# Optimization experiments

Measured on AMD Instinct MI355X. Metric: run time of the kernel, lower is better.

Reference implementation:

```python
import jax, jax.numpy as jnp
import numpy as np

H2 = 1.0  # self.bandwidth = bandwidth**2 with bandwidth=1.0

Q, N, D = 4096, 65536, 32


def setup_inputs() -> dict:
    key = jax.random.key(0)
    k1, k2, k3 = jax.random.split(key, 3)
    X = jax.random.normal(k1, (Q, D), dtype=jnp.float32)
    X_train = jax.random.normal(k2, (N, D), dtype=jnp.float32)
    sample_weight = jax.random.uniform(k3, (N,), dtype=jnp.float32)  # non-negative
    return {"X": X, "X_train": X_train, "sample_weight": sample_weight}


def reference(X, X_train, sample_weight):
    # Brute-force ('standard'/RootTree) KDE: every query sees all train points.
    d = X.shape[-1]
    d2 = (jnp.sum(X * X, axis=-1, keepdims=True)
          + jnp.sum(X_train * X_train, axis=-1)[None, :]
          - 2.0 * (X @ X_train.T))
    # GaussianKernel(diff) = (2*pi)^{-d/2} exp(-||diff||^2 / (2*H2))
    log_k = -0.5 * d2 / H2 - 0.5 * d * jnp.log(jnp.float32(2.0 * np.pi))
    # log( sum_j w_j K_ij / (bw_norm * sum_j w_j) ), bw_norm = H2**(d/2)
    log_num = jax.scipy.special.logsumexp(log_k + jnp.log(sample_weight)[None, :], axis=-1)
    log_norm = 0.5 * d * jnp.log(jnp.float32(H2)) + jnp.log(jnp.sum(sample_weight))
    return log_num - log_norm
```

## Files before the change

kernel.cpp:

```cpp
#include <hip/hip_runtime.h>
#include <math.h>

#define QN 4096
#define NN 65536
#define DD 32

typedef __attribute__((ext_vector_type(8))) _Float16 half8;
typedef __attribute__((ext_vector_type(4))) _Float16 half4v;
typedef __attribute__((ext_vector_type(4))) float floatx4;

#define LOG2E 1.4426950408889634f
#define HALF_D_LOG_2PI 29.40603306254953f

#define ASCALE 2954.6394357789634f
#define BSCALE 4096.0f
#define BIAS_F 1065353216.0f
#define CAPF   1585446912.0f
#define CENTER 0.970656f

__device__ __forceinline__ float fexp_term(float v) {
    v = __builtin_fminf(__builtin_fmaxf(v, 0.0f), CAPF);
    return __int_as_float((int)v);
}


__global__ __launch_bounds__(256) void prep_all(
    const float* __restrict__ X, const float* __restrict__ Xt,
    const float* __restrict__ w, _Float16* __restrict__ Xh,
    float* __restrict__ qn, _Float16* __restrict__ Xth,
    float* __restrict__ c, float* __restrict__ sumw) {
    const int b = blockIdx.x;
    if (b < 128) {
        int tid  = b * 256 + threadIdx.x;
        int row  = tid >> 3;
        int part = tid & 7;
        const float4 v = ((const float4*)X)[row * 8 + part];
        float nrm = v.x * v.x + v.y * v.y + v.z * v.z + v.w * v.w;
        nrm += __shfl_xor(nrm, 1);
        nrm += __shfl_xor(nrm, 2);
        nrm += __shfl_xor(nrm, 4);
        half4v h = { (_Float16)(v.x * ASCALE), (_Float16)(v.y * ASCALE),
                     (_Float16)(v.z * ASCALE), (_Float16)(v.w * ASCALE) };
        *(half4v*)(Xh + row * DD + part * 4) = h;
        if (part == 0) qn[row] = 0.5f * nrm;
    } else if (b < 2176) {
        int tid  = (b - 128) * 256 + threadIdx.x;
        int row  = tid >> 3;
        int part = tid & 7;
        const float4 v = ((const float4*)Xt)[row * 8 + part];
        float nrm = v.x * v.x + v.y * v.y + v.z * v.z + v.w * v.w;
        nrm += __shfl_xor(nrm, 1);
        nrm += __shfl_xor(nrm, 2);
        nrm += __shfl_xor(nrm, 4);
        half4v h = { (_Float16)(v.x * BSCALE), (_Float16)(v.y * BSCALE),
                     (_Float16)(v.z * BSCALE), (_Float16)(v.w * BSCALE) };
        *(half4v*)(Xth + row * DD + part * 4) = h;
        if (part == 0)
            c[row] = w[row] * __builtin_amdgcn_exp2f(-0.5f * LOG2E * nrm) * CENTER;
    } else {
        int bid = b - 2176;
        float v = 0.f;
        for (int i = bid * 256 + threadIdx.x; i < NN; i += 64 * 256)
            v += w[i];
        #pragma unroll
        for (int o = 1; o < 64; o <<= 1) v += __shfl_xor(v, o);
        __shared__ float red[4];
        if ((threadIdx.x & 63) == 0) red[threadIdx.x >> 6] = v;
        __syncthreads();
        if (threadIdx.x == 0) atomicAdd(sumw, red[0] + red[1] + red[2] + red[3]);
    }
}

__global__ __launch_bounds__(256) void kde_main(
    const _Float16* __restrict__ Xh, const _Float16* __restrict__ Xth,
    const float* __restrict__ c, float* __restrict__ S) {
    const int lane   = threadIdx.x & 63;
    const int wave   = threadIdx.x >> 6;
    const int quad   = lane >> 4;
    const int l16    = lane & 15;
    const int m_base = blockIdx.x * 256 + wave * 64;
    const int n_beg  = blockIdx.y * 512;

    half8 a0 = *(const half8*)(Xh + (m_base +  0 + l16) * DD + quad * 8);
    half8 a1 = *(const half8*)(Xh + (m_base + 16 + l16) * DD + quad * 8);
    half8 a2 = *(const half8*)(Xh + (m_base + 32 + l16) * DD + quad * 8);
    half8 a3 = *(const half8*)(Xh + (m_base + 48 + l16) * DD + quad * 8);

    float s0[4][4] = {};
    float s1[4][4] = {};
    const floatx4 cbias = {BIAS_F, BIAS_F, BIAS_F, BIAS_F};

    const _Float16* bp = Xth + (size_t)(n_beg + l16) * DD + quad * 8;
    const float*    cp = c + n_beg + l16;

    for (int it = 0; it < 16; ++it) {
        half8 b0 = *(const half8*)bp;
        half8 b1 = *(const half8*)(bp + 16 * DD);
        float c0 = cp[0];
        float c1 = cp[16];
        bp += 32 * DD;
        cp += 32;

        floatx4 g00 = __builtin_amdgcn_mfma_f32_16x16x32_f16(a0, b0, cbias, 0, 0, 0);
        floatx4 g10 = __builtin_amdgcn_mfma_f32_16x16x32_f16(a0, b1, cbias, 0, 0, 0);
        floatx4 g01 = __builtin_amdgcn_mfma_f32_16x16x32_f16(a1, b0, cbias, 0, 0, 0);
        floatx4 g11 = __builtin_amdgcn_mfma_f32_16x16x32_f16(a1, b1, cbias, 0, 0, 0);
        floatx4 g02 = __builtin_amdgcn_mfma_f32_16x16x32_f16(a2, b0, cbias, 0, 0, 0);
        floatx4 g12 = __builtin_amdgcn_mfma_f32_16x16x32_f16(a2, b1, cbias, 0, 0, 0);
        floatx4 g03 = __builtin_amdgcn_mfma_f32_16x16x32_f16(a3, b0, cbias, 0, 0, 0);
        floatx4 g13 = __builtin_amdgcn_mfma_f32_16x16x32_f16(a3, b1, cbias, 0, 0, 0);

        #pragma unroll
        for (int r = 0; r < 4; ++r) {
            s0[0][r] += c0 * fexp_term(g00[r]);
            s1[0][r] += c1 * fexp_term(g10[r]);
            s0[1][r] += c0 * fexp_term(g01[r]);
            s1[1][r] += c1 * fexp_term(g11[r]);
            s0[2][r] += c0 * fexp_term(g02[r]);
            s1[2][r] += c1 * fexp_term(g12[r]);
            s0[3][r] += c0 * fexp_term(g03[r]);
            s1[3][r] += c1 * fexp_term(g13[r]);
        }
    }

    #pragma unroll
    for (int t = 0; t < 4; ++t) {
        #pragma unroll
        for (int r = 0; r < 4; ++r) {
            float v = (t == 0 ? s0[0][r] + s1[0][r] :
                       t == 1 ? s0[1][r] + s1[1][r] :
                       t == 2 ? s0[2][r] + s1[2][r] :
                                s0[3][r] + s1[3][r]);
            v += __shfl_xor(v, 1);
            v += __shfl_xor(v, 2);
            v += __shfl_xor(v, 4);
            v += __shfl_xor(v, 8);
            if (l16 == 0)
                atomicAdd(&S[m_base + t * 16 + quad * 4 + r], v);
        }
    }
}

__global__ void finalize(const float* __restrict__ S, const float* __restrict__ qn,
                         const float* __restrict__ sumw, float* __restrict__ out) {
    int i = blockIdx.x * blockDim.x + threadIdx.x;
    out[i] = logf(S[i]) - qn[i] - HALF_D_LOG_2PI - logf(*sumw);
}

extern "C" void kernel_launch(void* const* d_in, const int* in_sizes, int n_in,
                              void* d_out, int out_size, void* d_ws, size_t ws_size,
                              hipStream_t stream) {
    const float* X  = (const float*)d_in[0];
    const float* Xt = (const float*)d_in[1];
    const float* w  = (const float*)d_in[2];
    float* out = (float*)d_out;

    char* ws = (char*)d_ws;
    _Float16* Xh   = (_Float16*)(ws);
    _Float16* Xth  = (_Float16*)(ws + 262144);
    float*    c    = (float*)(ws + 4456448);
    float*    qn   = (float*)(ws + 4718592);
    float*    S    = (float*)(ws + 4734976);
    float*    sumw = (float*)(ws + 4751360);

    hipMemsetAsync(S, 0, QN * sizeof(float) + sizeof(float), stream);

    prep_all<<<2240, 256, 0, stream>>>(X, Xt, w, Xh, qn, Xth, c, sumw);
    kde_main<<<dim3(QN / 256, 128), 256, 0, stream>>>(Xh, Xth, c, S);
    finalize<<<QN / 256, 256, 0, stream>>>(S, qn, sumw, out);
}
```

Baseline: 118.5 us.

## Drop memset, replace weight-sum atomic, remap blocks per XCD, prefetch B tiles

```diff
diff --git a/kernel.cpp b/kernel.cpp
--- a/kernel.cpp
+++ b/kernel.cpp
@@ -19,7 +19,7 @@
 #define CENTER 0.970656f
 
 __device__ __forceinline__ float fexp_term(float v) {
-    v = __builtin_fminf(__builtin_fmaxf(v, 0.0f), CAPF);
+    v = __builtin_amdgcn_fmed3f(v, 0.0f, CAPF);
     return __int_as_float((int)v);
 }
 
@@ -28,7 +28,8 @@
     const float* __restrict__ X, const float* __restrict__ Xt,
     const float* __restrict__ w, _Float16* __restrict__ Xh,
     float* __restrict__ qn, _Float16* __restrict__ Xth,
-    float* __restrict__ c, float* __restrict__ sumw) {
+    float* __restrict__ c, float* __restrict__ S,
+    float* __restrict__ swp) {
     const int b = blockIdx.x;
     if (b < 128) {
         int tid  = b * 256 + threadIdx.x;
@@ -43,6 +44,7 @@
                      (_Float16)(v.z * ASCALE), (_Float16)(v.w * ASCALE) };
         *(half4v*)(Xh + row * DD + part * 4) = h;
         if (part == 0) qn[row] = 0.5f * nrm;
+        if (tid < QN) S[tid] = 0.f;
     } else if (b < 2176) {
         int tid  = (b - 128) * 256 + threadIdx.x;
         int row  = tid >> 3;
@@ -67,7 +69,7 @@
         __shared__ float red[4];
         if ((threadIdx.x & 63) == 0) red[threadIdx.x >> 6] = v;
         __syncthreads();
-        if (threadIdx.x == 0) atomicAdd(sumw, red[0] + red[1] + red[2] + red[3]);
+        if (threadIdx.x == 0) swp[bid] = red[0] + red[1] + red[2] + red[3];
     }
 }
 
@@ -78,8 +80,14 @@
     const int wave   = threadIdx.x >> 6;
     const int quad   = lane >> 4;
     const int l16    = lane & 15;
-    const int m_base = blockIdx.x * 256 + wave * 64;
-    const int n_beg  = blockIdx.y * 512;
+
+    const int b      = blockIdx.x;
+    const int xcd    = b & 7;
+    const int slot   = b >> 3;
+    const int qx     = slot & 15;
+    const int strip  = xcd + 8 * (slot >> 4);
+    const int m_base = qx * 256 + wave * 64;
+    const int n_beg  = strip * 512;
 
     half8 a0 = *(const half8*)(Xh + (m_base +  0 + l16) * DD + quad * 8);
     half8 a1 = *(const half8*)(Xh + (m_base + 16 + l16) * DD + quad * 8);
@@ -93,13 +101,18 @@
     const _Float16* bp = Xth + (size_t)(n_beg + l16) * DD + quad * 8;
     const float*    cp = c + n_beg + l16;
 
+    half8 b0 = *(const half8*)bp;
+    half8 b1 = *(const half8*)(bp + 16 * DD);
+    float c0 = cp[0];
+    float c1 = cp[16];
+
     for (int it = 0; it < 16; ++it) {
-        half8 b0 = *(const half8*)bp;
-        half8 b1 = *(const half8*)(bp + 16 * DD);
-        float c0 = cp[0];
-        float c1 = cp[16];
         bp += 32 * DD;
         cp += 32;
+        half8 nb0 = *(const half8*)bp;
+        half8 nb1 = *(const half8*)(bp + 16 * DD);
+        float nc0 = cp[0];
+        float nc1 = cp[16];
 
         floatx4 g00 = __builtin_amdgcn_mfma_f32_16x16x32_f16(a0, b0, cbias, 0, 0, 0);
         floatx4 g10 = __builtin_amdgcn_mfma_f32_16x16x32_f16(a0, b1, cbias, 0, 0, 0);
@@ -121,6 +134,8 @@
             s0[3][r] += c0 * fexp_term(g03[r]);
             s1[3][r] += c1 * fexp_term(g13[r]);
         }
+
+        b0 = nb0; b1 = nb1; c0 = nc0; c1 = nc1;
     }
 
     #pragma unroll
@@ -142,9 +157,17 @@
 }
 
 __global__ void finalize(const float* __restrict__ S, const float* __restrict__ qn,
-                         const float* __restrict__ sumw, float* __restrict__ out) {
+                         const float* __restrict__ swp, float* __restrict__ out) {
+    float pv = swp[threadIdx.x & 63];
+    pv += __shfl_xor(pv, 1);
+    pv += __shfl_xor(pv, 2);
+    pv += __shfl_xor(pv, 4);
+    pv += __shfl_xor(pv, 8);
+    pv += __shfl_xor(pv, 16);
+    pv += __shfl_xor(pv, 32);
+    float lsw = logf(pv);
     int i = blockIdx.x * blockDim.x + threadIdx.x;
-    out[i] = logf(S[i]) - qn[i] - HALF_D_LOG_2PI - logf(*sumw);
+    out[i] = logf(S[i]) - qn[i] - HALF_D_LOG_2PI - lsw;
 }
 
 extern "C" void kernel_launch(void* const* d_in, const int* in_sizes, int n_in,
@@ -161,11 +184,9 @@
     float*    c    = (float*)(ws + 4456448);
     float*    qn   = (float*)(ws + 4718592);
     float*    S    = (float*)(ws + 4734976);
-    float*    sumw = (float*)(ws + 4751360);
+    float*    swp  = (float*)(ws + 4751360);
 
-    hipMemsetAsync(S, 0, QN * sizeof(float) + sizeof(float), stream);
-
-    prep_all<<<2240, 256, 0, stream>>>(X, Xt, w, Xh, qn, Xth, c, sumw);
-    kde_main<<<dim3(QN / 256, 128), 256, 0, stream>>>(Xh, Xth, c, S);
-    finalize<<<QN / 256, 256, 0, stream>>>(S, qn, sumw, out);
+    prep_all<<<2240, 256, 0, stream>>>(X, Xt, w, Xh, qn, Xth, c, S, swp);
+    kde_main<<<2048, 256, 0, stream>>>(Xh, Xth, c, S);
+    finalize<<<QN / 256, 256, 0, stream>>>(S, qn, swp, out);
 }
```

Measured after the change: 111.6 us. 1.06x faster.
